# Optimization experiments

Measured on AMD Instinct MI355X. Metric: run time of the kernel, lower is better.

## Reference

```python
import jax, jax.numpy as jnp
import numpy as np

THRESHOLD = 0.95
B, T, H = 32, 2000, 512
NUM_TARGETS = 250.0  # alphas normalized so each row sums to this (mimics alpha *= num/_num)
MAX_LABEL_LEN = 256


def setup_inputs() -> dict:
    key = jax.random.key(0)
    k1, k2 = jax.random.split(key)
    hidden = jax.random.normal(k1, (B, T, H), dtype=jnp.float32)
    u = jax.random.uniform(k2, (B, T), dtype=jnp.float32)
    alphas = u / u.sum(-1, keepdims=True) * NUM_TARGETS  # per-row sum == NUM_TARGETS
    return {"hidden": hidden, "alphas": alphas, "max_label_len": MAX_LABEL_LEN}


def _cif(hidden, alphas, max_label_len, threshold=THRESHOLD):
    """Continuous integrate-and-fire: sequential scan over time + fire-gather."""
    Bn, Tn, Hn = hidden.shape

    def step(carry, inp):
        integrate, frame = carry              # [B], [B, H]
        alpha, h = inp                        # [B], [B, H]
        dist_completion = 1.0 - integrate
        integ = integrate + alpha
        fire = integ > threshold              # [B] bool
        cur = jnp.where(fire, dist_completion, alpha)
        remainds = alpha - cur
        frame_out = frame + cur[:, None] * h  # emitted frame at this step
        integ_next = jnp.where(fire, integ - 1.0, integ)
        frame_next = jnp.where(fire[:, None], remainds[:, None] * h, frame_out)
        return (integ_next, frame_next), (integ, frame_out)

    init = (jnp.zeros((Bn,), hidden.dtype), jnp.zeros((Bn, Hn), hidden.dtype))
    xs = (jnp.swapaxes(alphas, 0, 1), jnp.swapaxes(hidden, 0, 1))  # time-major
    _, (fires_t, frames_t) = jax.lax.scan(step, init, xs)
    fires = jnp.swapaxes(fires_t, 0, 1)    # [B, T]
    frames = jnp.swapaxes(frames_t, 0, 1)  # [B, T, H]

    # Gather fired frames per batch row, left-packed and zero-padded to max_label_len.
    mask = fires > threshold                               # [B, T]
    pos = jnp.cumsum(mask.astype(jnp.int32), axis=1) - 1   # running fire index
    pos = jnp.where(mask, pos, max_label_len)              # non-fires go to dump slot
    out = jnp.zeros((Bn, max_label_len + 1, Hn), hidden.dtype)
    out = out.at[jnp.arange(Bn)[:, None], pos].set(frames)
    return out[:, :max_label_len]  # drop dump slot -> [B, L, H]


def reference(hidden, alphas, max_label_len):
    return _cif(hidden, alphas, max_label_len)
```

## Files before the change

kernel.cpp:

```cpp
#include <hip/hip_runtime.h>
#include <stdint.h>

static constexpr int   Bn      = 32;
static constexpr int   Tn      = 2000;
static constexpr int   Hn      = 512;
static constexpr int   Ln      = 256;
static constexpr float kThresh = 0.95f;
static constexpr int   TCHUNK  = 40;
static constexpr int   NTCH    = Tn / TCHUNK;
static constexpr int   MSTRIDE = 64;
static constexpr unsigned PUBF = 0x40000000u;

__global__ __launch_bounds__(64, 1) void cif_fused_kernel(
    const float* __restrict__ hidden,
    const float* __restrict__ alphas,
    uint64_t* __restrict__ meta,
    float* __restrict__ out) {
  const int lane = threadIdx.x;
  __shared__ __align__(16) float alds[Tn + 64];

  if (blockIdx.x < Bn) {
    __builtin_amdgcn_s_setprio(3);
    const int b = blockIdx.x;
    {
      const float4* __restrict__ arow =
          reinterpret_cast<const float4*>(alphas + (size_t)b * Tn);
      for (int i = lane; i < Tn / 4; i += 64)
        *reinterpret_cast<float4*>(&alds[4 * i]) = arow[i];
      for (int i = Tn / 4 + lane; i < (Tn + 64) / 4; i += 64)
        *reinterpret_cast<float4*>(&alds[4 * i]) =
            make_float4(0.f, 0.f, 0.f, 0.f);
    }
    __syncthreads();

    const float4* __restrict__ lds4 =
        reinterpret_cast<const float4*>(&alds[0]);
    float I  = 0.0f;
    int   fc = 0;

    float4 q0 = lds4[0], q1 = lds4[1], q2 = lds4[2], q3 = lds4[3],
           q4 = lds4[4];
    int rd = 5;

    auto step4 = [&](const float4& q) {
#pragma unroll
      for (int j = 0; j < 4; ++j) {
        const float a = (j == 0) ? q.x : (j == 1) ? q.y : (j == 2) ? q.z : q.w;
        const float integ = I + a;
        const bool  fire  = integ > kThresh;
        I  = fire ? (integ - 1.0f) : integ;
        fc += fire ? 1 : 0;
      }
    };

    for (int c = 0; c < 100; ++c) {
      if (lane == 0 && (c & 1) == 0) {
        const uint64_t v = ((uint64_t)__float_as_uint(I) << 32) |
                           (uint64_t)(PUBF | (unsigned)fc);
        __hip_atomic_store(&meta[(size_t)b * MSTRIDE + (c >> 1)], v,
                           __ATOMIC_RELAXED, __HIP_MEMORY_SCOPE_AGENT);
      }
      step4(q0); q0 = lds4[rd + 0];
      step4(q1); q1 = lds4[rd + 1];
      step4(q2); q2 = lds4[rd + 2];
      step4(q3); q3 = lds4[rd + 3];
      step4(q4); q4 = lds4[rd + 4];
      rd += 5;
    }
    return;
  }

  const int idx = blockIdx.x - Bn;
  const int b   = idx & (Bn - 1);
  const int tc  = idx >> 5;
  const int t_start = tc * TCHUNK;
  const int col = lane * 8;

  auto wait_meta = [&](int c) -> uint64_t {
    const uint64_t* p = &meta[(size_t)b * MSTRIDE + c];
    uint64_t v;
    for (;;) {
      v = __hip_atomic_load(p, __ATOMIC_RELAXED, __HIP_MEMORY_SCOPE_AGENT);
      if ((unsigned)v & PUBF) break;
      __builtin_amdgcn_s_sleep(16);
    }
    return v;
  };

  const float* __restrict__ arow = alphas + (size_t)b * Tn;

  float I; int s;
  if (tc == 0) { I = 0.0f; s = 0; }
  else {
    const uint64_t v = wait_meta(tc);
    I = __uint_as_float((unsigned)(v >> 32));
    s = (int)((unsigned)v & 0xFFFFu);
  }

  int   t_prev   = -1;
  float rem_prev = 0.0f;
  for (int k = 1; tc - k >= 0 && t_prev < 0; ++k) {
    const int ck = tc - k;
    float Ik;
    if (ck == 0) Ik = 0.0f;
    else {
      const uint64_t v = wait_meta(ck);
      Ik = __uint_as_float((unsigned)(v >> 32));
    }
    const float* __restrict__ ap = arow + ck * TCHUNK;
    int lt = -1; float lrem = 0.0f;
#pragma unroll
    for (int j = 0; j < TCHUNK; ++j) {
      const float a     = ap[j];
      const float integ = Ik + a;
      const bool  fire  = integ > kThresh;
      if (fire) { lt = ck * TCHUNK + j; lrem = a - (1.0f - Ik); }
      Ik = fire ? (integ - 1.0f) : integ;
    }
    if (lt >= 0) { t_prev = lt; rem_prev = lrem; }
  }

  const float* __restrict__ hb = hidden + (size_t)b * Tn * Hn + col;
  float4 acc0 = make_float4(0.f, 0.f, 0.f, 0.f);
  float4 acc1 = make_float4(0.f, 0.f, 0.f, 0.f);
  float4 h0, h1;

  auto loadh = [&](int t) {
    h0 = *reinterpret_cast<const float4*>(hb + (size_t)t * Hn);
    h1 = *reinterpret_cast<const float4*>(hb + (size_t)t * Hn + 4);
  };
  auto acc8 = [&](float wt) {
    acc0.x += wt * h0.x; acc0.y += wt * h0.y;
    acc0.z += wt * h0.z; acc0.w += wt * h0.w;
    acc1.x += wt * h1.x; acc1.y += wt * h1.y;
    acc1.z += wt * h1.z; acc1.w += wt * h1.w;
  };
  auto set8 = [&](float wt) {
    acc0.x = wt * h0.x; acc0.y = wt * h0.y;
    acc0.z = wt * h0.z; acc0.w = wt * h0.w;
    acc1.x = wt * h1.x; acc1.y = wt * h1.y;
    acc1.z = wt * h1.z; acc1.w = wt * h1.w;
  };

  if (t_prev >= 0) {
    loadh(t_prev);
    set8(rem_prev);
  }
  for (int t = t_prev + 1; t < t_start; ++t) {
    loadh(t);
    acc8(arow[t]);
  }

  for (int j = 0; j < TCHUNK; ++j) {
    const int   t     = t_start + j;
    const float a     = arow[t];
    const float integ = I + a;
    const bool  fire  = integ > kThresh;
    loadh(t);
    if (fire) {
      const float cw = 1.0f - I;
      acc8(cw);
      if (s < Ln) {
        float* op = out + ((size_t)b * Ln + s) * Hn + col;
        *reinterpret_cast<float4*>(op)     = acc0;
        *reinterpret_cast<float4*>(op + 4) = acc1;
      }
      const float rem = a - cw;
      set8(rem);
      s += 1;
      I  = integ - 1.0f;
    } else {
      acc8(a);
      I = integ;
    }
  }
  if (tc == NTCH - 1) {
    const float4 z = make_float4(0.f, 0.f, 0.f, 0.f);
    for (int s2 = s; s2 < Ln; ++s2) {
      float* op = out + ((size_t)b * Ln + s2) * Hn + col;
      *reinterpret_cast<float4*>(op)     = z;
      *reinterpret_cast<float4*>(op + 4) = z;
    }
  }
}

extern "C" void kernel_launch(void* const* d_in, const int* in_sizes, int n_in,
                              void* d_out, int out_size, void* d_ws, size_t ws_size,
                              hipStream_t stream) {
  const float* hidden = (const float*)d_in[0];
  const float* alphas = (const float*)d_in[1];
  float* out = (float*)d_out;

  uint64_t* meta = (uint64_t*)d_ws;
  hipMemsetAsync(meta, 0, (size_t)Bn * MSTRIDE * sizeof(uint64_t), stream);

  const int nblocks = Bn + NTCH * Bn;
  cif_fused_kernel<<<nblocks, 64, 0, stream>>>(hidden, alphas, meta, out);
}
```

Baseline: 64.99 us.

## Halve time chunk size and software-prefetch next hidden row in fire loop

Halves the time chunk size to 20, doubling the number of worker blocks per batch row. The scan block now publishes its integrator state every 20 steps instead of every 40, so workers can start sooner. The per-chunk loop also prefetches the next hidden row one step ahead, hiding load latency behind the accumulate. The cost is more blocks, more metadata stores and polling, and more lookback work to find the previous fire.

```diff
diff --git a/kernel.cpp b/kernel.cpp
--- a/kernel.cpp
+++ b/kernel.cpp
@@ -6,9 +6,9 @@
 static constexpr int   Hn      = 512;
 static constexpr int   Ln      = 256;
 static constexpr float kThresh = 0.95f;
-static constexpr int   TCHUNK  = 40;
+static constexpr int   TCHUNK  = 20;
 static constexpr int   NTCH    = Tn / TCHUNK;
-static constexpr int   MSTRIDE = 64;
+static constexpr int   MSTRIDE = 128;
 static constexpr unsigned PUBF = 0x40000000u;
 
 __global__ __launch_bounds__(64, 1) void cif_fused_kernel(
@@ -54,10 +54,10 @@
     };
 
     for (int c = 0; c < 100; ++c) {
-      if (lane == 0 && (c & 1) == 0) {
+      if (lane == 0) {
         const uint64_t v = ((uint64_t)__float_as_uint(I) << 32) |
                            (uint64_t)(PUBF | (unsigned)fc);
-        __hip_atomic_store(&meta[(size_t)b * MSTRIDE + (c >> 1)], v,
+        __hip_atomic_store(&meta[(size_t)b * MSTRIDE + c], v,
                            __ATOMIC_RELAXED, __HIP_MEMORY_SCOPE_AGENT);
       }
       step4(q0); q0 = lds4[rd + 0];
@@ -123,56 +123,68 @@
   const float* __restrict__ hb = hidden + (size_t)b * Tn * Hn + col;
   float4 acc0 = make_float4(0.f, 0.f, 0.f, 0.f);
   float4 acc1 = make_float4(0.f, 0.f, 0.f, 0.f);
-  float4 h0, h1;
-
-  auto loadh = [&](int t) {
-    h0 = *reinterpret_cast<const float4*>(hb + (size_t)t * Hn);
-    h1 = *reinterpret_cast<const float4*>(hb + (size_t)t * Hn + 4);
+
+  auto loadh0 = [&](int t) -> float4 {
+    return *reinterpret_cast<const float4*>(hb + (size_t)t * Hn);
   };
-  auto acc8 = [&](float wt) {
-    acc0.x += wt * h0.x; acc0.y += wt * h0.y;
-    acc0.z += wt * h0.z; acc0.w += wt * h0.w;
-    acc1.x += wt * h1.x; acc1.y += wt * h1.y;
-    acc1.z += wt * h1.z; acc1.w += wt * h1.w;
+  auto loadh1 = [&](int t) -> float4 {
+    return *reinterpret_cast<const float4*>(hb + (size_t)t * Hn + 4);
   };
-  auto set8 = [&](float wt) {
-    acc0.x = wt * h0.x; acc0.y = wt * h0.y;
-    acc0.z = wt * h0.z; acc0.w = wt * h0.w;
-    acc1.x = wt * h1.x; acc1.y = wt * h1.y;
-    acc1.z = wt * h1.z; acc1.w = wt * h1.w;
-  };
 
   if (t_prev >= 0) {
-    loadh(t_prev);
-    set8(rem_prev);
+    const float4 h0 = loadh0(t_prev);
+    const float4 h1 = loadh1(t_prev);
+    acc0.x = rem_prev * h0.x; acc0.y = rem_prev * h0.y;
+    acc0.z = rem_prev * h0.z; acc0.w = rem_prev * h0.w;
+    acc1.x = rem_prev * h1.x; acc1.y = rem_prev * h1.y;
+    acc1.z = rem_prev * h1.z; acc1.w = rem_prev * h1.w;
   }
   for (int t = t_prev + 1; t < t_start; ++t) {
-    loadh(t);
-    acc8(arow[t]);
-  }
-
+    const float a   = arow[t];
+    const float4 h0 = loadh0(t);
+    const float4 h1 = loadh1(t);
+    acc0.x += a * h0.x; acc0.y += a * h0.y;
+    acc0.z += a * h0.z; acc0.w += a * h0.w;
+    acc1.x += a * h1.x; acc1.y += a * h1.y;
+    acc1.z += a * h1.z; acc1.w += a * h1.w;
+  }
+
+  float4 c0 = loadh0(t_start);
+  float4 c1 = loadh1(t_start);
   for (int j = 0; j < TCHUNK; ++j) {
-    const int   t     = t_start + j;
+    const int t  = t_start + j;
+    const int tn = (j + 1 < TCHUNK) ? t + 1 : t;
+    const float4 n0 = loadh0(tn);
+    const float4 n1 = loadh1(tn);
     const float a     = arow[t];
     const float integ = I + a;
     const bool  fire  = integ > kThresh;
-    loadh(t);
     if (fire) {
       const float cw = 1.0f - I;
-      acc8(cw);
+      acc0.x += cw * c0.x; acc0.y += cw * c0.y;
+      acc0.z += cw * c0.z; acc0.w += cw * c0.w;
+      acc1.x += cw * c1.x; acc1.y += cw * c1.y;
+      acc1.z += cw * c1.z; acc1.w += cw * c1.w;
       if (s < Ln) {
         float* op = out + ((size_t)b * Ln + s) * Hn + col;
         *reinterpret_cast<float4*>(op)     = acc0;
         *reinterpret_cast<float4*>(op + 4) = acc1;
       }
       const float rem = a - cw;
-      set8(rem);
+      acc0.x = rem * c0.x; acc0.y = rem * c0.y;
+      acc0.z = rem * c0.z; acc0.w = rem * c0.w;
+      acc1.x = rem * c1.x; acc1.y = rem * c1.y;
+      acc1.z = rem * c1.z; acc1.w = rem * c1.w;
       s += 1;
       I  = integ - 1.0f;
     } else {
-      acc8(a);
+      acc0.x += a * c0.x; acc0.y += a * c0.y;
+      acc0.z += a * c0.z; acc0.w += a * c0.w;
+      acc1.x += a * c1.x; acc1.y += a * c1.y;
+      acc1.z += a * c1.z; acc1.w += a * c1.w;
       I = integ;
     }
+    c0 = n0; c1 = n1;
   }
   if (tc == NTCH - 1) {
     const float4 z = make_float4(0.f, 0.f, 0.f, 0.f);
```

Measured after the change: 54.28 us, median of 2. 1.2x faster.
